# Kernel tuning notes

Measured on AMD Instinct MI355X. Metric: run time of the kernel, lower is better.

## Reference

```python
import jax, jax.numpy as jnp
import numpy as np

DIM = 1024
HEADS = 16
DK = DIM // HEADS
B, LQ, LKV = 2, 2048, 2048


def setup_inputs() -> dict:
    key = jax.random.key(0)
    ks = jax.random.split(key, 12)
    s = 1.0 / np.sqrt(DIM)
    return {
        "output": jax.random.normal(ks[0], (B, LQ, DIM), jnp.float32),
        "context": jax.random.normal(ks[1], (B, LKV, DIM), jnp.float32),
        # torch nn.Linear(dim, dim): store as [in, out] so y = x @ W + b
        "Wq": jax.random.normal(ks[2], (DIM, DIM), jnp.float32) * s,
        "bq": jax.random.normal(ks[3], (DIM,), jnp.float32) * s,
        "Wk": jax.random.normal(ks[4], (DIM, DIM), jnp.float32) * s,
        "bk": jax.random.normal(ks[5], (DIM,), jnp.float32) * s,
        "Wv": jax.random.normal(ks[6], (DIM, DIM), jnp.float32) * s,
        "bv": jax.random.normal(ks[7], (DIM,), jnp.float32) * s,
        # linear_out: in = 2*dim, out = dim
        "Wo": jax.random.normal(ks[8], (2 * DIM, DIM), jnp.float32) * (1.0 / np.sqrt(2 * DIM)),
        "bo": jax.random.normal(ks[9], (DIM,), jnp.float32) * (1.0 / np.sqrt(2 * DIM)),
    }


def _to_batches(x):
    # [B, L, dim] -> [B*H, L, dk], same layout as the torch reshape/permute
    b, l, _ = x.shape
    return x.reshape(b, l, HEADS, DK).transpose(0, 2, 1, 3).reshape(b * HEADS, l, DK)


def reference(output, context, Wq, bq, Wk, bk, Wv, bv, Wo, bo):
    b, lq, dim = output.shape
    q = _to_batches(output @ Wq + bq)     # [B*H, Lq, dk]
    k = _to_batches(context @ Wk + bk)    # [B*H, Lkv, dk]
    v = _to_batches(context @ Wv + bv)    # [B*H, Lkv, dk]

    scores = jnp.einsum('bqd,bkd->bqk', q, k) / jnp.sqrt(jnp.asarray(DK, q.dtype))
    attn = jax.nn.softmax(scores, axis=-1)            # [B*H, Lq, Lkv]; dropout = identity at eval
    ctx = jnp.einsum('bqk,bkd->bqd', attn, v)          # [B*H, Lq, dk]

    # Faithful to the original (non-standard) reshape:
    # scores.transpose(1,2).contiguous().view(B, -1, dim)
    concat = ctx.transpose(0, 2, 1).reshape(b, -1, dim)  # [B, Lq, dim] (permuted layout)
    combined = jnp.concatenate([concat, output], axis=2)  # [B, Lq, 2*dim]
    out = jnp.tanh(combined @ Wo + bo)                     # [B, Lq, dim]
    return (out, attn)
```

## Files before the change

kernel.cpp:

```cpp
#include <hip/hip_runtime.h>
#include <math.h>
#include <stdint.h>

#define DIM_ 1024
#define HEADS_ 16
#define DK_ 64
#define B_ 2
#define L_ 2048
#define BH_ (B_*HEADS_)
#define M_ (B_*L_)

typedef __attribute__((ext_vector_type(4))) float f32x4;
typedef __attribute__((ext_vector_type(8))) short bf16x8;
typedef __attribute__((ext_vector_type(4))) short bf16x4;

#define QSCALE 0.18033688f

static __device__ __forceinline__ short f2bf(float f) {
    uint32_t u = __builtin_bit_cast(uint32_t, f);
    u += 0x7fffu + ((u >> 16) & 1u);
    return (short)(u >> 16);
}
static __device__ __forceinline__ float bf2f(short h) {
    uint32_t u = ((uint32_t)(unsigned short)h) << 16;
    return __builtin_bit_cast(float, u);
}
static __device__ __forceinline__ void gload16(const void* g, void* l) {
    __builtin_amdgcn_global_load_lds(
        (const __attribute__((address_space(1))) unsigned int*)g,
        (__attribute__((address_space(3))) unsigned int*)l, 16, 0, 0);
}

__global__ __launch_bounds__(256)
void cvt_bf16(const float* __restrict__ a, const float* __restrict__ b,
              short* __restrict__ ao, short* __restrict__ bo)
{
    const int id = blockIdx.x * 256 + threadIdx.x;
    const int nA = (M_ * DIM_) / 8;
    const float* src = (id < nA) ? a : b;
    short* dst = (id < nA) ? ao : bo;
    const int c = (id < nA) ? id : id - nA;
    const f32x4 v0 = *(const f32x4*)&src[(size_t)c * 8];
    const f32x4 v1 = *(const f32x4*)&src[(size_t)c * 8 + 4];
    bf16x8 o;
#pragma unroll
    for (int i = 0; i < 4; ++i) { o[i] = f2bf(v0[i]); o[4 + i] = f2bf(v1[i]); }
    *(bf16x8*)&dst[(size_t)c * 8] = o;
}

__global__ __launch_bounds__(256)
void wtrans(const float* __restrict__ Wq, const float* __restrict__ Wk,
            const float* __restrict__ Wv, const float* __restrict__ Wo,
            short* __restrict__ WqT, short* __restrict__ WkT,
            short* __restrict__ WvT, short* __restrict__ WoT)
{
    const int z = blockIdx.z;
    const int K = (z == 3) ? 2 * DIM_ : DIM_;
    const int k0 = blockIdx.x * 64;
    if (k0 >= K) return;
    const int n0 = blockIdx.y * 64;
    const float* W = (z == 0) ? Wq : (z == 1) ? Wk : (z == 2) ? Wv : Wo;
    short* WT = (z == 0) ? WqT : (z == 1) ? WkT : (z == 2) ? WvT : WoT;

    __shared__ float ts[64][65];
    const int tid = threadIdx.x;
    {
        const int k = tid >> 2, noff = (tid & 3) * 16;
#pragma unroll
        for (int i = 0; i < 4; ++i)
            *(f32x4*)&ts[k][noff + i * 4] =
                *(const f32x4*)&W[(size_t)(k0 + k) * DIM_ + n0 + noff + i * 4];
    }
    __syncthreads();
    {
        const int n = tid >> 2, koff = (tid & 3) * 16;
#pragma unroll
        for (int c = 0; c < 2; ++c) {
            bf16x8 o;
#pragma unroll
            for (int i = 0; i < 8; ++i) o[i] = f2bf(ts[koff + c * 8 + i][n]);
            *(bf16x8*)&WT[(size_t)(n0 + n) * K + k0 + koff + c * 8] = o;
        }
    }
}

__global__ __launch_bounds__(256)
void qkv_mfma(const short* __restrict__ xoutb, const short* __restrict__ xctxb,
              const short* __restrict__ WqT, const short* __restrict__ WkT,
              const short* __restrict__ WvT,
              const float* __restrict__ bq, const float* __restrict__ bk,
              const float* __restrict__ bv,
              short* __restrict__ qh, short* __restrict__ kh, short* __restrict__ vT)
{
    const int z = blockIdx.z;
    const short* A  = (z == 0) ? xoutb : xctxb;
    const short* Bt = (z == 0) ? WqT : (z == 1) ? WkT : WvT;
    const float* bias = (z == 0) ? bq : (z == 1) ? bk : bv;

    const int flat = blockIdx.y * 8 + blockIdx.x;
    const int wgs = (flat & 7) * 32 + (flat >> 3);
    const int col0 = (wgs & 7) * 128;
    const int row0 = (wgs >> 3) * 128;
    const int tid = threadIdx.x;
    const int lane = tid & 63;
    const int w = tid >> 6;
    const int wm = (w >> 1) * 64, wn = (w & 1) * 64;
    const int l15 = lane & 15, g = lane >> 4;
    const int sub = lane >> 3, slt = lane & 7;

    __shared__ short As[128 * 64];
    __shared__ short Bs[128 * 64];

    const short* pA[4]; const short* pB[4]; short* ldsA[4]; short* ldsB[4];
#pragma unroll
    for (int i = 0; i < 4; ++i) {
        const int r = w * 32 + i * 8 + sub;
        const int sc = ((slt ^ (r & 7)) * 8);
        pA[i] = A  + (size_t)(row0 + r) * DIM_ + sc;
        pB[i] = Bt + (size_t)(col0 + r) * DIM_ + sc;
        ldsA[i] = &As[(w * 32 + i * 8) * 64];
        ldsB[i] = &Bs[(w * 32 + i * 8) * 64];
    }

    f32x4 acc[4][4];
#pragma unroll
    for (int mi = 0; mi < 4; ++mi)
#pragma unroll
        for (int ni = 0; ni < 4; ++ni) acc[mi][ni] = (f32x4)0.f;

    for (int k0 = 0; k0 < DIM_; k0 += 64) {
#pragma unroll
        for (int i = 0; i < 4; ++i) {
            gload16(pA[i] + k0, ldsA[i]);
            gload16(pB[i] + k0, ldsB[i]);
        }
        __syncthreads();
        bf16x8 af[4][2], bfr[4][2];
#pragma unroll
        for (int mi = 0; mi < 4; ++mi) {
            const int wa = wm + mi * 16 + l15;
#pragma unroll
            for (int ks = 0; ks < 2; ++ks)
                af[mi][ks] = *(const bf16x8*)&As[wa * 64 + (((ks * 4 + g) ^ (wa & 7)) * 8)];
        }
#pragma unroll
        for (int ni = 0; ni < 4; ++ni) {
            const int wb = wn + ni * 16 + l15;
#pragma unroll
            for (int ks = 0; ks < 2; ++ks)
                bfr[ni][ks] = *(const bf16x8*)&Bs[wb * 64 + (((ks * 4 + g) ^ (wb & 7)) * 8)];
        }
        __builtin_amdgcn_s_setprio(1);
#pragma unroll
        for (int mi = 0; mi < 4; ++mi)
#pragma unroll
            for (int ni = 0; ni < 4; ++ni)
#pragma unroll
                for (int ks = 0; ks < 2; ++ks)
                    acc[mi][ni] = __builtin_amdgcn_mfma_f32_16x16x32_bf16(af[mi][ks], bfr[ni][ks], acc[mi][ni], 0, 0, 0);
        __builtin_amdgcn_s_setprio(0);
        __syncthreads();
    }

#pragma unroll
    for (int ni = 0; ni < 4; ++ni) {
        const int col = col0 + wn + ni * 16 + l15;
        const int h = col >> 6, dk = col & 63;
        const float bb = bias[col];
#pragma unroll
        for (int mi = 0; mi < 4; ++mi) {
            const int rowb = row0 + wm + mi * 16 + g * 4;
            const int b = rowb >> 11;
            const int l = rowb & (L_ - 1);
            const int bh = b * 16 + h;
            if (z == 2) {
                bf16x4 o;
#pragma unroll
                for (int r = 0; r < 4; ++r) o[r] = f2bf(acc[mi][ni][r] + bb);
                *(bf16x4*)&vT[(size_t)(bh * 64 + dk) * L_ + l] = o;
            } else {
                short* dst = (z == 0) ? qh : kh;
                const float sc = (z == 0) ? QSCALE : 1.0f;
#pragma unroll
                for (int r = 0; r < 4; ++r)
                    dst[((size_t)bh * L_ + l + r) * DK_ + dk] = f2bf((acc[mi][ni][r] + bb) * sc);
            }
        }
    }
}

__global__ __launch_bounds__(512, 8)
void attn_mfma(const short* __restrict__ qh, const short* __restrict__ kh,
               const short* __restrict__ vT,
               float* __restrict__ attn, short* __restrict__ ctxTb)
{
    const int bid = blockIdx.x;
    const int wg = (bid & 7) * 128 + (bid >> 3);
    const int bh = wg >> 5;
    const int q0 = (wg & 31) * 64;

    const int tid = threadIdx.x;
    const int lane = tid & 63;
    const int w = tid >> 6;
    const int wq = w >> 1, wk = w & 1;
    const int l15 = lane & 15, g = lane >> 4;

    __shared__ short Kb0[64 * 64];
    __shared__ short Kb1[64 * 64];
    __shared__ short Vb[64 * 64];
    __shared__ short Psb[64 * 72];
    __shared__ float stat[4][2][16][2];

    const short* kbase = kh + (size_t)bh * (L_ * DK_);
    const short* vbase = vT + (size_t)bh * (DK_ * L_);

    const int lr = lane >> 3, ls = lane & 7;
    const int srow = w * 8 + lr;
    const short* kSrc = kbase + (size_t)srow * DK_ + ((ls ^ (srow & 7)) * 8);
    const short* vSrc = vbase + (size_t)srow * L_ + ((ls ^ (srow & 7)) * 8);
    short* kDst0 = &Kb0[w * 512];
    short* kDst1 = &Kb1[w * 512];
    short* vDst  = &Vb[w * 512];

    bf16x8 qf[2];
#pragma unroll
    for (int ks = 0; ks < 2; ++ks)
        qf[ks] = *(const bf16x8*)&qh[((size_t)bh * L_ + q0 + wq * 16 + l15) * DK_ + ks * 32 + g * 8];

    int kbOff[2][2], vbOff[4];
#pragma unroll
    for (int cc = 0; cc < 2; ++cc)
#pragma unroll
        for (int ks = 0; ks < 2; ++ks) {
            const int row = wk * 32 + cc * 16 + l15;
            kbOff[cc][ks] = row * 64 + (((ks * 4 + g) ^ (row & 7)) * 8);
        }
#pragma unroll
    for (int nf = 0; nf < 4; ++nf) {
        const int row = nf * 16 + l15;
        vbOff[nf] = row * 64 + (((wk * 4 + g) ^ (row & 7)) * 8);
    }

    float m[4], s[4];
#pragma unroll
    for (int r = 0; r < 4; ++r) { m[r] = -1e30f; s[r] = 0.f; }

    gload16(kSrc, kDst0);
    __syncthreads();
    for (int t = 0; t < 32; ++t) {
        if (t < 31) gload16(kSrc + (size_t)(t + 1) * 64 * DK_, (t & 1) ? kDst0 : kDst1);
        const short* kb = (t & 1) ? Kb1 : Kb0;
        f32x4 sa[2];
#pragma unroll
        for (int cc = 0; cc < 2; ++cc) sa[cc] = (f32x4)0.f;
        __builtin_amdgcn_s_setprio(1);
#pragma unroll
        for (int cc = 0; cc < 2; ++cc)
#pragma unroll
            for (int ks = 0; ks < 2; ++ks)
                sa[cc] = __builtin_amdgcn_mfma_f32_16x16x32_bf16(qf[ks], *(const bf16x8*)&kb[kbOff[cc][ks]], sa[cc], 0, 0, 0);
        __builtin_amdgcn_s_setprio(0);
#pragma unroll
        for (int r = 0; r < 4; ++r) {
            const float tm = fmaxf(sa[0][r], sa[1][r]);
            const float mn = fmaxf(m[r], tm);
            s[r] = s[r] * exp2f(m[r] - mn) + exp2f(sa[0][r] - mn) + exp2f(sa[1][r] - mn);
            m[r] = mn;
        }
        __syncthreads();
    }
#pragma unroll
    for (int mask = 1; mask <= 8; mask <<= 1) {
#pragma unroll
        for (int r = 0; r < 4; ++r) {
            const float mo = __shfl_xor(m[r], mask);
            const float so = __shfl_xor(s[r], mask);
            const float mn = fmaxf(m[r], mo);
            s[r] = s[r] * exp2f(m[r] - mn) + so * exp2f(mo - mn);
            m[r] = mn;
        }
    }
    if (l15 == 0) {
#pragma unroll
        for (int r = 0; r < 4; ++r) {
            stat[wq][wk][g * 4 + r][0] = m[r];
            stat[wq][wk][g * 4 + r][1] = s[r];
        }
    }
    gload16(kSrc, kDst0);
    __syncthreads();
    float inv_s[4];
#pragma unroll
    for (int r = 0; r < 4; ++r) {
        const float m0 = stat[wq][0][g * 4 + r][0], s0 = stat[wq][0][g * 4 + r][1];
        const float m1 = stat[wq][1][g * 4 + r][0], s1 = stat[wq][1][g * 4 + r][1];
        const float mn = fmaxf(m0, m1);
        m[r] = mn;
        inv_s[r] = 1.0f / (s0 * exp2f(m0 - mn) + s1 * exp2f(m1 - mn));
    }

    f32x4 cacc[4];
#pragma unroll
    for (int nf = 0; nf < 4; ++nf) cacc[nf] = (f32x4)0.f;

    float* attnB = attn + ((size_t)bh * L_ + q0) * L_;
    const int arow = tid >> 3, acol = (tid & 7) * 8;

    for (int t = 0; t < 32; ++t) {
        if (t < 31) gload16(kSrc + (size_t)(t + 1) * 64 * DK_, (t & 1) ? kDst0 : kDst1);
        gload16(vSrc + t * 64, vDst);
        const short* kb = (t & 1) ? Kb1 : Kb0;
        f32x4 sa[2];
#pragma unroll
        for (int cc = 0; cc < 2; ++cc) sa[cc] = (f32x4)0.f;
        __builtin_amdgcn_s_setprio(1);
#pragma unroll
        for (int cc = 0; cc < 2; ++cc)
#pragma unroll
            for (int ks = 0; ks < 2; ++ks)
                sa[cc] = __builtin_amdgcn_mfma_f32_16x16x32_bf16(qf[ks], *(const bf16x8*)&kb[kbOff[cc][ks]], sa[cc], 0, 0, 0);
        __builtin_amdgcn_s_setprio(0);
#pragma unroll
        for (int cc = 0; cc < 2; ++cc)
#pragma unroll
            for (int r = 0; r < 4; ++r)
                Psb[(wq * 16 + g * 4 + r) * 72 + wk * 32 + cc * 16 + l15] =
                    f2bf(exp2f(sa[cc][r] - m[r]) * inv_s[r]);
        __syncthreads();
        {
            const bf16x8 pv = *(const bf16x8*)&Psb[arow * 72 + acol];
            float* dst = attnB + (size_t)arow * L_ + t * 64 + acol;
            f32x4 o0, o1;
#pragma unroll
            for (int i = 0; i < 4; ++i) { o0[i] = bf2f(pv[i]); o1[i] = bf2f(pv[4 + i]); }
            __builtin_nontemporal_store(o0, (f32x4*)dst);
            __builtin_nontemporal_store(o1, (f32x4*)(dst + 4));
        }
        const bf16x8 pa = *(const bf16x8*)&Psb[(wq * 16 + l15) * 72 + wk * 32 + g * 8];
        __builtin_amdgcn_s_setprio(1);
#pragma unroll
        for (int nf = 0; nf < 4; ++nf)
            cacc[nf] = __builtin_amdgcn_mfma_f32_16x16x32_bf16(pa, *(const bf16x8*)&Vb[vbOff[nf]], cacc[nf], 0, 0, 0);
        __builtin_amdgcn_s_setprio(0);
        __syncthreads();
    }

    float* scr = (float*)&Kb0[0];
    float* scr1 = (float*)&Kb1[0];
    if (wk) {
#pragma unroll
        for (int nf = 0; nf < 4; ++nf) {
            float* p = (nf < 2) ? scr : scr1;
            *(f32x4*)&p[(((wq * 2) + (nf & 1)) * 64 + lane) * 4] = cacc[nf];
        }
    }
    __syncthreads();
    if (!wk) {
#pragma unroll
        for (int nf = 0; nf < 4; ++nf) {
            const float* p = (nf < 2) ? scr : scr1;
            const f32x4 o = cacc[nf] + *(const f32x4*)&p[(((wq * 2) + (nf & 1)) * 64 + lane) * 4];
            bf16x4 ob;
#pragma unroll
            for (int r = 0; r < 4; ++r) ob[r] = f2bf(o[r]);
            *(bf16x4*)&ctxTb[(size_t)(bh * 64 + nf * 16 + l15) * L_ + q0 + wq * 16 + g * 4] = ob;
        }
    }
}

__global__ __launch_bounds__(256)
void out_mfma(const short* __restrict__ ctxTb, const short* __restrict__ xoutb,
              const short* __restrict__ WoT, const float* __restrict__ bo,
              float* __restrict__ out)
{
    const int flat = blockIdx.y * 16 + blockIdx.x;
    const int wgs = (flat & 7) * 64 + (flat >> 3);
    const int col0 = (wgs & 15) * 64;
    const int row0 = (wgs >> 4) * 128;
    const int tid = threadIdx.x;
    const int lane = tid & 63;
    const int w = tid >> 6;
    const int wm = (w >> 1) * 64, wn = (w & 1) * 32;
    const int l15 = lane & 15, g = lane >> 4;
    const int sub = lane >> 3, slt = lane & 7;

    __shared__ short As[128 * 64];
    __shared__ short Bs[64 * 64];

    const short* pA1[4]; const short* pA2[4]; const short* pB[2];
    short* ldsA[4]; short* ldsB[2];
#pragma unroll
    for (int i = 0; i < 4; ++i) {
        const int r = w * 32 + i * 8 + sub;
        const int rr = row0 + r;
        const int b = rr >> 11, l_ = rr & (L_ - 1);
        const int bh = b * 16 + (l_ >> 7), d = (l_ & 127) >> 1;
        const size_t off1 = ((size_t)(bh * 64 + d) << 11) + (size_t)((l_ & 1) << 10);
        const int sc = ((slt ^ (r & 7)) * 8);
        pA1[i] = ctxTb + off1 + sc;
        pA2[i] = xoutb + (size_t)rr * DIM_ + sc;
        ldsA[i] = &As[(w * 32 + i * 8) * 64];
    }
#pragma unroll
    for (int i = 0; i < 2; ++i) {
        const int r = w * 16 + i * 8 + sub;
        const int sc = ((slt ^ (r & 7)) * 8);
        pB[i]  = WoT + (size_t)(col0 + r) * (2 * DIM_) + sc;
        ldsB[i] = &Bs[(w * 16 + i * 8) * 64];
    }

    f32x4 acc[4][2];
#pragma unroll
    for (int mi = 0; mi < 4; ++mi)
#pragma unroll
        for (int ni = 0; ni < 2; ++ni) acc[mi][ni] = (f32x4)0.f;

    for (int k0 = 0; k0 < 2 * DIM_; k0 += 64) {
        const bool first = (k0 < DIM_);
        const int kk = first ? k0 : k0 - DIM_;
#pragma unroll
        for (int i = 0; i < 4; ++i)
            gload16(first ? (pA1[i] + kk) : (pA2[i] + kk), ldsA[i]);
#pragma unroll
        for (int i = 0; i < 2; ++i)
            gload16(pB[i] + k0, ldsB[i]);
        __syncthreads();
        bf16x8 af[4][2], bfr[2][2];
#pragma unroll
        for (int mi = 0; mi < 4; ++mi) {
            const int wa = wm + mi * 16 + l15;
#pragma unroll
            for (int ks = 0; ks < 2; ++ks)
                af[mi][ks] = *(const bf16x8*)&As[wa * 64 + (((ks * 4 + g) ^ (wa & 7)) * 8)];
        }
#pragma unroll
        for (int ni = 0; ni < 2; ++ni) {
            const int wb = wn + ni * 16 + l15;
#pragma unroll
            for (int ks = 0; ks < 2; ++ks)
                bfr[ni][ks] = *(const bf16x8*)&Bs[wb * 64 + (((ks * 4 + g) ^ (wb & 7)) * 8)];
        }
        __builtin_amdgcn_s_setprio(1);
#pragma unroll
        for (int mi = 0; mi < 4; ++mi)
#pragma unroll
            for (int ni = 0; ni < 2; ++ni)
#pragma unroll
                for (int ks = 0; ks < 2; ++ks)
                    acc[mi][ni] = __builtin_amdgcn_mfma_f32_16x16x32_bf16(af[mi][ks], bfr[ni][ks], acc[mi][ni], 0, 0, 0);
        __builtin_amdgcn_s_setprio(0);
        __syncthreads();
    }

#pragma unroll
    for (int ni = 0; ni < 2; ++ni) {
        const int col = col0 + wn + ni * 16 + l15;
        const float bb = bo[col];
#pragma unroll
        for (int mi = 0; mi < 4; ++mi) {
            const int rowb = row0 + wm + mi * 16 + g * 4;
#pragma unroll
            for (int r = 0; r < 4; ++r)
                out[(size_t)(rowb + r) * DIM_ + col] = tanhf(acc[mi][ni][r] + bb);
        }
    }
}

extern "C" void kernel_launch(void* const* d_in, const int* in_sizes, int n_in,
                              void* d_out, int out_size, void* d_ws, size_t ws_size,
                              hipStream_t stream)
{
    const float* xout = (const float*)d_in[0];
    const float* xctx = (const float*)d_in[1];
    const float* Wq = (const float*)d_in[2];
    const float* bq = (const float*)d_in[3];
    const float* Wk = (const float*)d_in[4];
    const float* bk = (const float*)d_in[5];
    const float* Wv = (const float*)d_in[6];
    const float* bv = (const float*)d_in[7];
    const float* Wo = (const float*)d_in[8];
    const float* bo = (const float*)d_in[9];

    float* out  = (float*)d_out;
    float* attn = out + (size_t)M_ * DIM_;

    short* ws = (short*)d_ws;
    short* xoutb = ws;
    short* xctxb = xoutb + (size_t)M_ * DIM_;
    short* WqT   = xctxb + (size_t)M_ * DIM_;
    short* WkT   = WqT + (size_t)DIM_ * DIM_;
    short* WvT   = WkT + (size_t)DIM_ * DIM_;
    short* WoT   = WvT + (size_t)DIM_ * DIM_;
    short* qh    = WoT + (size_t)2 * DIM_ * DIM_;
    short* kh    = qh + (size_t)BH_ * L_ * DK_;
    short* vT    = kh + (size_t)BH_ * L_ * DK_;
    short* ctxTb = vT + (size_t)BH_ * L_ * DK_;

    cvt_bf16<<<(2 * M_ * DIM_ / 8) / 256, 256, 0, stream>>>(xout, xctx, xoutb, xctxb);
    wtrans<<<dim3(32, 16, 4), 256, 0, stream>>>(Wq, Wk, Wv, Wo, WqT, WkT, WvT, WoT);
    qkv_mfma<<<dim3(8, 32, 3), 256, 0, stream>>>(
        xoutb, xctxb, WqT, WkT, WvT, bq, bk, bv, qh, kh, vT);
    attn_mfma<<<1024, 512, 0, stream>>>(qh, kh, vT, attn, ctxTb);
    out_mfma<<<dim3(16, 32), 256, 0, stream>>>(ctxTb, xoutb, WoT, bo, out);
}
```

Baseline: 338.0 us.

## Replace syncthreads with manual vmcnt waits and write attn directly from registers

New measurement: 283.7 us. -16.1%, faster.

```diff
diff --git a/kernel.cpp b/kernel.cpp
--- a/kernel.cpp
+++ b/kernel.cpp
@@ -246,8 +246,15 @@
     for (int r = 0; r < 4; ++r) { m[r] = -1e30f; s[r] = 0.f; }
 
     gload16(kSrc, kDst0);
-    __syncthreads();
+    asm volatile("s_waitcnt vmcnt(0)" ::: "memory");
+    __builtin_amdgcn_sched_barrier(0);
+    __builtin_amdgcn_s_barrier();
     for (int t = 0; t < 32; ++t) {
+        if (t) {
+            asm volatile("s_waitcnt vmcnt(0)" ::: "memory");
+            __builtin_amdgcn_sched_barrier(0);
+            __builtin_amdgcn_s_barrier();
+        }
         if (t < 31) gload16(kSrc + (size_t)(t + 1) * 64 * DK_, (t & 1) ? kDst0 : kDst1);
         const short* kb = (t & 1) ? Kb1 : Kb0;
         f32x4 sa[2];
@@ -267,7 +274,6 @@
             s[r] = s[r] * exp2f(m[r] - mn) + exp2f(sa[0][r] - mn) + exp2f(sa[1][r] - mn);
             m[r] = mn;
         }
-        __syncthreads();
     }
 #pragma unroll
     for (int mask = 1; mask <= 8; mask <<= 1) {
@@ -288,7 +294,8 @@
         }
     }
     gload16(kSrc, kDst0);
-    __syncthreads();
+    asm volatile("s_waitcnt lgkmcnt(0)" ::: "memory");
+    __builtin_amdgcn_s_barrier();
     float inv_s[4];
 #pragma unroll
     for (int r = 0; r < 4; ++r) {
@@ -304,11 +311,22 @@
     for (int nf = 0; nf < 4; ++nf) cacc[nf] = (f32x4)0.f;
 
     float* attnB = attn + ((size_t)bh * L_ + q0) * L_;
-    const int arow = tid >> 3, acol = (tid & 7) * 8;
+
+    asm volatile("s_waitcnt vmcnt(0)" ::: "memory");
+    __builtin_amdgcn_sched_barrier(0);
+    __builtin_amdgcn_s_barrier();
 
     for (int t = 0; t < 32; ++t) {
-        if (t < 31) gload16(kSrc + (size_t)(t + 1) * 64 * DK_, (t & 1) ? kDst0 : kDst1);
+        if (t) {
+            asm volatile("s_waitcnt vmcnt(8)" ::: "memory");
+            __builtin_amdgcn_sched_barrier(0);
+            __builtin_amdgcn_s_barrier();
+        }
         gload16(vSrc + t * 64, vDst);
+        {
+            const int tn = (t < 31) ? t + 1 : t;
+            gload16(kSrc + (size_t)tn * 64 * DK_, (t & 1) ? kDst0 : kDst1);
+        }
         const short* kb = (t & 1) ? Kb1 : Kb0;
         f32x4 sa[2];
 #pragma unroll
@@ -323,28 +341,24 @@
 #pragma unroll
         for (int cc = 0; cc < 2; ++cc)
 #pragma unroll
-            for (int r = 0; r < 4; ++r)
-                Psb[(wq * 16 + g * 4 + r) * 72 + wk * 32 + cc * 16 + l15] =
-                    f2bf(exp2f(sa[cc][r] - m[r]) * inv_s[r]);
-        __syncthreads();
-        {
-            const bf16x8 pv = *(const bf16x8*)&Psb[arow * 72 + acol];
-            float* dst = attnB + (size_t)arow * L_ + t * 64 + acol;
-            f32x4 o0, o1;
-#pragma unroll
-            for (int i = 0; i < 4; ++i) { o0[i] = bf2f(pv[i]); o1[i] = bf2f(pv[4 + i]); }
-            __builtin_nontemporal_store(o0, (f32x4*)dst);
-            __builtin_nontemporal_store(o1, (f32x4*)(dst + 4));
-        }
+            for (int r = 0; r < 4; ++r) {
+                const float p = exp2f(sa[cc][r] - m[r]) * inv_s[r];
+                Psb[(wq * 16 + g * 4 + r) * 72 + wk * 32 + cc * 16 + l15] = f2bf(p);
+                __builtin_nontemporal_store(
+                    p, attnB + (size_t)(wq * 16 + g * 4 + r) * L_ + t * 64 + wk * 32 + cc * 16 + l15);
+            }
+        asm volatile("s_waitcnt vmcnt(9) lgkmcnt(0)" ::: "memory");
+        __builtin_amdgcn_sched_barrier(0);
+        __builtin_amdgcn_s_barrier();
         const bf16x8 pa = *(const bf16x8*)&Psb[(wq * 16 + l15) * 72 + wk * 32 + g * 8];
         __builtin_amdgcn_s_setprio(1);
 #pragma unroll
         for (int nf = 0; nf < 4; ++nf)
             cacc[nf] = __builtin_amdgcn_mfma_f32_16x16x32_bf16(pa, *(const bf16x8*)&Vb[vbOff[nf]], cacc[nf], 0, 0, 0);
         __builtin_amdgcn_s_setprio(0);
-        __syncthreads();
-    }
-
+    }
+
+    __syncthreads();
     float* scr = (float*)&Kb0[0];
     float* scr1 = (float*)&Kb1[0];
     if (wk) {
```
